# Kernel tuning notes

Measured on AMD Instinct MI355X. Metric: run time of the kernel, lower is better.

Reference implementation:

```python
import jax, jax.numpy as jnp
import numpy as np

N = 1_000_000   # pose-graph nodes
E = 2_000_000   # edges (odometry + loop closures)
M = N - 1
L1, L2, L3, L4 = 1.0, 0.1, 1.0, 0.1  # loss weights
EPS = 1e-8

# ---- quaternion / Lie-group helpers (pypose convention: [x,y,z,w]) ----

def qmul(q, r):
    qv, qw = q[..., :3], q[..., 3:]
    rv, rw = r[..., :3], r[..., 3:]
    w = qw * rw - jnp.sum(qv * rv, axis=-1, keepdims=True)
    v = qw * rv + rw * qv + jnp.cross(qv, rv)
    return jnp.concatenate([v, w], axis=-1)

def qconj(q):  # inverse of a unit quaternion
    return jnp.concatenate([-q[..., :3], q[..., 3:]], axis=-1)

def qrot(q, v):  # rotate vector v by unit quaternion q
    qv, qw = q[..., :3], q[..., 3:]
    t = 2.0 * jnp.cross(qv, v)
    return v + qw * t + jnp.cross(qv, t)

def so3_log(q):  # SO3 -> so3 rotation vector phi
    v, w = q[..., :3], q[..., 3]
    n = jnp.linalg.norm(v, axis=-1)
    theta = 2.0 * jnp.arctan2(n, w)
    big = n > EPS
    k = jnp.where(big, theta / jnp.where(big, n, 1.0), 2.0 / jnp.where(jnp.abs(w) > EPS, w, 1.0))
    return v * k[..., None]

def se3_log(t, q):  # SE3 -> se3 = [tau(3), phi(3)] (translation first, pypose order)
    phi = so3_log(q)
    theta2 = jnp.sum(phi * phi, axis=-1)
    theta = jnp.sqrt(theta2)
    small = theta < 1e-4
    ts = jnp.where(small, 1.0, theta)
    # V^{-1} coefficient: 1/theta^2 - (1+cos)/(2 theta sin); Taylor -> 1/12
    coef = jnp.where(small, 1.0 / 12.0,
                     1.0 / jnp.where(small, 1.0, theta2)
                     - (1.0 + jnp.cos(ts)) / (2.0 * ts * jnp.sin(ts)))
    pxt = jnp.cross(phi, t)
    tau = t - 0.5 * pxt + coef[..., None] * jnp.cross(phi, pxt)  # V^{-1} t without 3x3 mats
    return jnp.concatenate([tau, phi], axis=-1)

def _unit_quat(key, n):
    q = jax.random.normal(key, (n, 4), dtype=jnp.float32)
    return q / jnp.linalg.norm(q, axis=-1, keepdims=True)

def setup_inputs() -> dict:
    key = jax.random.key(0)
    k = jax.random.split(key, 9)
    nodes = jnp.concatenate([jax.random.normal(k[0], (N, 3), jnp.float32), _unit_quat(k[1], N)], axis=-1)
    vels = jax.random.normal(k[2], (N, 3), jnp.float32)
    edges = jax.random.randint(k[3], (E, 2), 0, N, dtype=jnp.int32)
    poses = jnp.concatenate([jax.random.normal(k[4], (E, 3), jnp.float32), _unit_quat(k[5], E)], axis=-1)
    imu_drots = _unit_quat(k[6], M)
    imu_dtrans = 0.1 * jax.random.normal(k[7], (M, 3), jnp.float32)
    imu_dvels = 0.1 * jax.random.normal(k[8], (M, 3), jnp.float32)
    dts = jnp.full((M, 1), 0.05, dtype=jnp.float32)
    return dict(edges=edges, nodes=nodes, vels=vels, poses=poses,
                imu_drots=imu_drots, imu_dtrans=imu_dtrans, imu_dvels=imu_dvels, dts=dts)

def reference(edges, nodes, vels, poses, imu_drots, imu_dtrans, imu_dvels, dts):
    t_n, q_n = nodes[:, :3], nodes[:, 3:]
    # --- pose-graph residual: (poses^-1 o node1^-1 o node2).Log() ---
    n1 = nodes[edges[:, 0]]
    n2 = nodes[edges[:, 1]]
    t1, q1 = n1[:, :3], n1[:, 3:]
    t2, q2 = n2[:, :3], n2[:, 3:]
    tp, qp = poses[:, :3], poses[:, 3:]
    qi1 = qconj(q1)
    ti1 = -qrot(qi1, t1)           # node1^-1
    qa = qmul(qi1, q2)
    ta = ti1 + qrot(qi1, t2)       # node1^-1 o node2
    qip = qconj(qp)
    tip = -qrot(qip, tp)           # poses^-1
    qe = qmul(qip, qa)
    te = tip + qrot(qip, ta)
    pgerr = se3_log(te, qe)                                   # [E, 6]
    # --- adjacent velocity residual ---
    adjvelerr = imu_dvels - (vels[1:] - vels[:-1])            # [M, 3]
    # --- IMU rotation residual: (drot^-1 o R1^-1 o R2).Log() ---
    qre = qmul(qconj(imu_drots), qmul(qconj(q_n[:-1]), q_n[1:]))
    imuroterr = so3_log(qre)                                  # [M, 3]
    # --- translation/velocity residual ---
    transvelerr = (t_n[1:] - t_n[:-1]) - (vels[:-1] * dts + imu_dtrans)  # [M, 3]
    return jnp.concatenate([L1 * pgerr.ravel(), L2 * adjvelerr.ravel(),
                            L3 * imuroterr.ravel(), L4 * transvelerr.ravel()], axis=0)
```

## Files before the change

### kernel.cpp

```cpp
#include <hip/hip_runtime.h>
#include <math.h>

#define EPS_Q 1e-8f

struct F3 { float x, y, z; };
struct Q4 { F3 v; float w; };

__device__ __forceinline__ F3 add3(F3 a, F3 b){ return {a.x+b.x, a.y+b.y, a.z+b.z}; }
__device__ __forceinline__ F3 sub3(F3 a, F3 b){ return {a.x-b.x, a.y-b.y, a.z-b.z}; }
__device__ __forceinline__ F3 scal3(float s, F3 a){ return {s*a.x, s*a.y, s*a.z}; }
__device__ __forceinline__ float dot3(F3 a, F3 b){ return a.x*b.x + a.y*b.y + a.z*b.z; }
__device__ __forceinline__ F3 cross3(F3 a, F3 b){
    return { a.y*b.z - a.z*b.y, a.z*b.x - a.x*b.z, a.x*b.y - a.y*b.x };
}
__device__ __forceinline__ Q4 qmul(Q4 q, Q4 r){
    Q4 o;
    o.w = q.w*r.w - dot3(q.v, r.v);
    o.v = add3(add3(scal3(q.w, r.v), scal3(r.w, q.v)), cross3(q.v, r.v));
    return o;
}
__device__ __forceinline__ Q4 qconj(Q4 q){ return { {-q.v.x, -q.v.y, -q.v.z}, q.w }; }
__device__ __forceinline__ F3 qrot(Q4 q, F3 v){
    F3 t = scal3(2.0f, cross3(q.v, v));
    return add3(add3(v, scal3(q.w, t)), cross3(q.v, t));
}
__device__ __forceinline__ F3 so3_log(Q4 q){
    float n = sqrtf(dot3(q.v, q.v));
    float theta = 2.0f * atan2f(n, q.w);
    float k;
    if (n > EPS_Q) k = theta / n;
    else           k = 2.0f / ((fabsf(q.w) > EPS_Q) ? q.w : 1.0f);
    return scal3(k, q.v);
}

__device__ __forceinline__ void edge_compute(F3 t1, Q4 q1, F3 t2, Q4 q2,
                                             F3 tp, Q4 qp, float* __restrict__ o)
{
    Q4 qi1 = qconj(q1);
    F3 ti1 = scal3(-1.0f, qrot(qi1, t1));
    Q4 qa  = qmul(qi1, q2);
    F3 ta  = add3(ti1, qrot(qi1, t2));

    Q4 qip = qconj(qp);
    F3 tip = scal3(-1.0f, qrot(qip, tp));
    Q4 qe  = qmul(qip, qa);
    F3 te  = add3(tip, qrot(qip, ta));

    F3 phi = so3_log(qe);
    float theta2 = dot3(phi, phi);
    float theta  = sqrtf(theta2);
    float coef;
    if (theta < 1e-4f) {
        coef = 1.0f / 12.0f;
    } else {
        coef = 1.0f / theta2 - (1.0f + cosf(theta)) / (2.0f * theta * sinf(theta));
    }
    F3 pxt = cross3(phi, te);
    F3 tau = add3(sub3(te, scal3(0.5f, pxt)), scal3(coef, cross3(phi, pxt)));

    __builtin_nontemporal_store(tau.x, o + 0);
    __builtin_nontemporal_store(tau.y, o + 1);
    __builtin_nontemporal_store(tau.z, o + 2);
    __builtin_nontemporal_store(phi.x, o + 3);
    __builtin_nontemporal_store(phi.y, o + 4);
    __builtin_nontemporal_store(phi.z, o + 5);
}

__global__ void pad_nodes_kernel(const float* __restrict__ nodes,
                                 float4* __restrict__ pn, int N)
{
    int i = blockIdx.x * blockDim.x + threadIdx.x;
    if (i >= N) return;
    const float* s = nodes + 7*(size_t)i;
    float4 a = { s[0], s[1], s[2], s[3] };
    float4 b = { s[4], s[5], s[6], 0.0f };
    pn[2*(size_t)i    ] = a;
    pn[2*(size_t)i + 1] = b;
}

__global__ void fused_main(const int*    __restrict__ edges,
                           const float4* __restrict__ pn,
                           const float*  __restrict__ poses,
                           const float*  __restrict__ vels,
                           const float*  __restrict__ imu_drots,
                           const float*  __restrict__ imu_dtrans,
                           const float*  __restrict__ imu_dvels,
                           const float*  __restrict__ dts,
                           float*        __restrict__ out,
                           int E, int M, int edge_threads)
{
    int tid = blockIdx.x * blockDim.x + threadIdx.x;
    if (tid < edge_threads) {
        int e0 = 2*tid;
        int e1 = e0 + 1;
        bool has1 = (e1 < E);
        int e1s = has1 ? e1 : e0;

        int i0 = __builtin_nontemporal_load(edges + 2*(size_t)e0);
        int j0 = __builtin_nontemporal_load(edges + 2*(size_t)e0 + 1);
        int i1 = __builtin_nontemporal_load(edges + 2*(size_t)e1s);
        int j1 = __builtin_nontemporal_load(edges + 2*(size_t)e1s + 1);

        float4 na0 = pn[2*(size_t)i0], na1 = pn[2*(size_t)i0 + 1];
        float4 nb0 = pn[2*(size_t)j0], nb1 = pn[2*(size_t)j0 + 1];
        float4 nc0 = pn[2*(size_t)i1], nc1 = pn[2*(size_t)i1 + 1];
        float4 nd0 = pn[2*(size_t)j1], nd1 = pn[2*(size_t)j1 + 1];

        const float* p0 = poses + 7*(size_t)e0;
        const float* p1 = poses + 7*(size_t)e1s;
        float pp0[7], pp1[7];
        #pragma unroll
        for (int k = 0; k < 7; ++k) pp0[k] = __builtin_nontemporal_load(p0 + k);
        #pragma unroll
        for (int k = 0; k < 7; ++k) pp1[k] = __builtin_nontemporal_load(p1 + k);

        {
            F3 t1 = {na0.x, na0.y, na0.z};  Q4 q1 = {{na0.w, na1.x, na1.y}, na1.z};
            F3 t2 = {nb0.x, nb0.y, nb0.z};  Q4 q2 = {{nb0.w, nb1.x, nb1.y}, nb1.z};
            F3 tp = {pp0[0], pp0[1], pp0[2]}; Q4 qp = {{pp0[3], pp0[4], pp0[5]}, pp0[6]};
            edge_compute(t1, q1, t2, q2, tp, qp, out + 6*(size_t)e0);
        }
        if (has1) {
            F3 t1 = {nc0.x, nc0.y, nc0.z};  Q4 q1 = {{nc0.w, nc1.x, nc1.y}, nc1.z};
            F3 t2 = {nd0.x, nd0.y, nd0.z};  Q4 q2 = {{nd0.w, nd1.x, nd1.y}, nd1.z};
            F3 tp = {pp1[0], pp1[1], pp1[2]}; Q4 qp = {{pp1[3], pp1[4], pp1[5]}, pp1[6]};
            edge_compute(t1, q1, t2, q2, tp, qp, out + 6*(size_t)e1);
        }
    } else {
        int m = tid - edge_threads;
        if (m >= M) return;

        const size_t off_adjvel   = 6*(size_t)E;
        const size_t off_imurot   = off_adjvel + 3*(size_t)M;
        const size_t off_transvel = off_imurot + 3*(size_t)M;

        float4 n0a = pn[2*(size_t)m    ], n0b = pn[2*(size_t)m + 1];
        float4 n1a = pn[2*(size_t)m + 2], n1b = pn[2*(size_t)m + 3];
        F3 t0 = {n0a.x, n0a.y, n0a.z};  Q4 q0 = {{n0a.w, n0b.x, n0b.y}, n0b.z};
        F3 t1 = {n1a.x, n1a.y, n1a.z};  Q4 q1 = {{n1a.w, n1b.x, n1b.y}, n1b.z};

        F3 v0 = {vels[3*(size_t)m],     vels[3*(size_t)m + 1], vels[3*(size_t)m + 2]};
        F3 v1 = {vels[3*(size_t)m + 3], vels[3*(size_t)m + 4], vels[3*(size_t)m + 5]};

        F3 dvm = { __builtin_nontemporal_load(imu_dvels + 3*(size_t)m),
                   __builtin_nontemporal_load(imu_dvels + 3*(size_t)m + 1),
                   __builtin_nontemporal_load(imu_dvels + 3*(size_t)m + 2) };
        F3 adjv = sub3(dvm, sub3(v1, v0));
        __builtin_nontemporal_store(0.1f * adjv.x, out + off_adjvel + 3*(size_t)m);
        __builtin_nontemporal_store(0.1f * adjv.y, out + off_adjvel + 3*(size_t)m + 1);
        __builtin_nontemporal_store(0.1f * adjv.z, out + off_adjvel + 3*(size_t)m + 2);

        const float4 drv = ((const float4*)imu_drots)[m];
        Q4 dr = {{drv.x, drv.y, drv.z}, drv.w};
        Q4 qre = qmul(qconj(dr), qmul(qconj(q0), q1));
        F3 rot = so3_log(qre);
        __builtin_nontemporal_store(rot.x, out + off_imurot + 3*(size_t)m);
        __builtin_nontemporal_store(rot.y, out + off_imurot + 3*(size_t)m + 1);
        __builtin_nontemporal_store(rot.z, out + off_imurot + 3*(size_t)m + 2);

        float dt = dts[m];
        F3 dtr = { __builtin_nontemporal_load(imu_dtrans + 3*(size_t)m),
                   __builtin_nontemporal_load(imu_dtrans + 3*(size_t)m + 1),
                   __builtin_nontemporal_load(imu_dtrans + 3*(size_t)m + 2) };
        F3 tv = sub3(sub3(t1, t0), add3(scal3(dt, v0), dtr));
        __builtin_nontemporal_store(0.1f * tv.x, out + off_transvel + 3*(size_t)m);
        __builtin_nontemporal_store(0.1f * tv.y, out + off_transvel + 3*(size_t)m + 1);
        __builtin_nontemporal_store(0.1f * tv.z, out + off_transvel + 3*(size_t)m + 2);
    }
}

__global__ void edge_kernel(const int*   __restrict__ edges,
                            const float* __restrict__ nodes,
                            const float* __restrict__ poses,
                            float*       __restrict__ out,
                            int E)
{
    int e = blockIdx.x * blockDim.x + threadIdx.x;
    if (e >= E) return;
    int i = edges[2*(size_t)e];
    int j = edges[2*(size_t)e + 1];
    const float* n1 = nodes + 7*(size_t)i;
    const float* n2 = nodes + 7*(size_t)j;
    const float* p  = poses + 7*(size_t)e;
    F3 t1 = {n1[0], n1[1], n1[2]};  Q4 q1 = {{n1[3], n1[4], n1[5]}, n1[6]};
    F3 t2 = {n2[0], n2[1], n2[2]};  Q4 q2 = {{n2[3], n2[4], n2[5]}, n2[6]};
    F3 tp = {p[0],  p[1],  p[2]};   Q4 qp = {{p[3],  p[4],  p[5]},  p[6]};
    edge_compute(t1, q1, t2, q2, tp, qp, out + 6*(size_t)e);
}

__global__ void node_kernel(const float* __restrict__ nodes,
                            const float* __restrict__ vels,
                            const float* __restrict__ imu_drots,
                            const float* __restrict__ imu_dtrans,
                            const float* __restrict__ imu_dvels,
                            const float* __restrict__ dts,
                            float*       __restrict__ out,
                            int M,
                            size_t off_adjvel, size_t off_imurot, size_t off_transvel)
{
    int m = blockIdx.x * blockDim.x + threadIdx.x;
    if (m >= M) return;
    const float* n0 = nodes + 7*(size_t)m;
    const float* n1 = nodes + 7*(size_t)(m+1);
    F3 t0 = {n0[0], n0[1], n0[2]};  Q4 q0 = {{n0[3], n0[4], n0[5]}, n0[6]};
    F3 t1 = {n1[0], n1[1], n1[2]};  Q4 q1 = {{n1[3], n1[4], n1[5]}, n1[6]};
    F3 v0 = {vels[3*(size_t)m],     vels[3*(size_t)m + 1], vels[3*(size_t)m + 2]};
    F3 v1 = {vels[3*(size_t)m + 3], vels[3*(size_t)m + 4], vels[3*(size_t)m + 5]};
    F3 dvm = {imu_dvels[3*(size_t)m], imu_dvels[3*(size_t)m + 1], imu_dvels[3*(size_t)m + 2]};
    F3 adjv = sub3(dvm, sub3(v1, v0));
    out[off_adjvel + 3*(size_t)m    ] = 0.1f * adjv.x;
    out[off_adjvel + 3*(size_t)m + 1] = 0.1f * adjv.y;
    out[off_adjvel + 3*(size_t)m + 2] = 0.1f * adjv.z;
    Q4 dr = {{imu_drots[4*(size_t)m], imu_drots[4*(size_t)m + 1], imu_drots[4*(size_t)m + 2]},
              imu_drots[4*(size_t)m + 3]};
    Q4 qre = qmul(qconj(dr), qmul(qconj(q0), q1));
    F3 rot = so3_log(qre);
    out[off_imurot + 3*(size_t)m    ] = rot.x;
    out[off_imurot + 3*(size_t)m + 1] = rot.y;
    out[off_imurot + 3*(size_t)m + 2] = rot.z;
    float dt = dts[m];
    F3 dtr = {imu_dtrans[3*(size_t)m], imu_dtrans[3*(size_t)m + 1], imu_dtrans[3*(size_t)m + 2]};
    F3 tv = sub3(sub3(t1, t0), add3(scal3(dt, v0), dtr));
    out[off_transvel + 3*(size_t)m    ] = 0.1f * tv.x;
    out[off_transvel + 3*(size_t)m + 1] = 0.1f * tv.y;
    out[off_transvel + 3*(size_t)m + 2] = 0.1f * tv.z;
}

extern "C" void kernel_launch(void* const* d_in, const int* in_sizes, int n_in,
                              void* d_out, int out_size, void* d_ws, size_t ws_size,
                              hipStream_t stream) {
    const int*   edges      = (const int*)  d_in[0];
    const float* nodes      = (const float*)d_in[1];
    const float* vels       = (const float*)d_in[2];
    const float* poses      = (const float*)d_in[3];
    const float* imu_drots  = (const float*)d_in[4];
    const float* imu_dtrans = (const float*)d_in[5];
    const float* imu_dvels  = (const float*)d_in[6];
    const float* dts        = (const float*)d_in[7];
    float* out = (float*)d_out;

    const int E = in_sizes[0] / 2;
    const int N = in_sizes[1] / 7;
    const int M = in_sizes[7];

    const int BLK = 256;
    const size_t need = 2 * (size_t)N * sizeof(float4);

    if (ws_size >= need) {
        float4* pn = (float4*)d_ws;
        pad_nodes_kernel<<<(N + BLK - 1) / BLK, BLK, 0, stream>>>(nodes, pn, N);
        const int edge_threads = (E + 1) / 2;
        const long long total = (long long)edge_threads + M;
        fused_main<<<(int)((total + BLK - 1) / BLK), BLK, 0, stream>>>(
            edges, pn, poses, vels, imu_drots, imu_dtrans, imu_dvels, dts,
            out, E, M, edge_threads);
    } else {
        const size_t off_adjvel   = 6*(size_t)E;
        const size_t off_imurot   = off_adjvel + 3*(size_t)M;
        const size_t off_transvel = off_imurot + 3*(size_t)M;
        edge_kernel<<<(E + BLK - 1) / BLK, BLK, 0, stream>>>(edges, nodes, poses, out, E);
        node_kernel<<<(M + BLK - 1) / BLK, BLK, 0, stream>>>(nodes, vels, imu_drots, imu_dtrans,
                                                             imu_dvels, dts, out, M,
                                                             off_adjvel, off_imurot, off_transvel);
    }
}
```

Before: 301.1 us.

## Split fused kernel, interleave edge pairs by half-stride, drop nontemporal hints

Replaces the fused edge/node kernel with separate edge and node kernels. Each edge thread now handles edges t and t+half, so adjacent threads read adjacent edge and pose records. Edge indices are loaded as int2. Nontemporal load and store hints are replaced with ordinary accesses. This aims for better coalescing and simpler per-kernel code, at the cost of an extra launch and possible cache pollution from the output stores.

After: 275.8 us. 8.4% less time.

```diff
diff --git a/kernel.cpp b/kernel.cpp
--- a/kernel.cpp
+++ b/kernel.cpp
@@ -58,12 +58,8 @@
     F3 pxt = cross3(phi, te);
     F3 tau = add3(sub3(te, scal3(0.5f, pxt)), scal3(coef, cross3(phi, pxt)));
 
-    __builtin_nontemporal_store(tau.x, o + 0);
-    __builtin_nontemporal_store(tau.y, o + 1);
-    __builtin_nontemporal_store(tau.z, o + 2);
-    __builtin_nontemporal_store(phi.x, o + 3);
-    __builtin_nontemporal_store(phi.y, o + 4);
-    __builtin_nontemporal_store(phi.z, o + 5);
+    o[0] = tau.x; o[1] = tau.y; o[2] = tau.z;
+    o[3] = phi.x; o[4] = phi.y; o[5] = phi.z;
 }
 
 __global__ void pad_nodes_kernel(const float* __restrict__ nodes,
@@ -78,95 +74,90 @@
     pn[2*(size_t)i + 1] = b;
 }
 
-__global__ void fused_main(const int*    __restrict__ edges,
-                           const float4* __restrict__ pn,
-                           const float*  __restrict__ poses,
-                           const float*  __restrict__ vels,
-                           const float*  __restrict__ imu_drots,
-                           const float*  __restrict__ imu_dtrans,
-                           const float*  __restrict__ imu_dvels,
-                           const float*  __restrict__ dts,
-                           float*        __restrict__ out,
-                           int E, int M, int edge_threads)
-{
-    int tid = blockIdx.x * blockDim.x + threadIdx.x;
-    if (tid < edge_threads) {
-        int e0 = 2*tid;
-        int e1 = e0 + 1;
-        bool has1 = (e1 < E);
-        int e1s = has1 ? e1 : e0;
-
-        int i0 = __builtin_nontemporal_load(edges + 2*(size_t)e0);
-        int j0 = __builtin_nontemporal_load(edges + 2*(size_t)e0 + 1);
-        int i1 = __builtin_nontemporal_load(edges + 2*(size_t)e1s);
-        int j1 = __builtin_nontemporal_load(edges + 2*(size_t)e1s + 1);
-
-        float4 na0 = pn[2*(size_t)i0], na1 = pn[2*(size_t)i0 + 1];
-        float4 nb0 = pn[2*(size_t)j0], nb1 = pn[2*(size_t)j0 + 1];
-        float4 nc0 = pn[2*(size_t)i1], nc1 = pn[2*(size_t)i1 + 1];
-        float4 nd0 = pn[2*(size_t)j1], nd1 = pn[2*(size_t)j1 + 1];
-
-        const float* p0 = poses + 7*(size_t)e0;
-        const float* p1 = poses + 7*(size_t)e1s;
-        float pp0[7], pp1[7];
-        #pragma unroll
-        for (int k = 0; k < 7; ++k) pp0[k] = __builtin_nontemporal_load(p0 + k);
-        #pragma unroll
-        for (int k = 0; k < 7; ++k) pp1[k] = __builtin_nontemporal_load(p1 + k);
-
-        {
-            F3 t1 = {na0.x, na0.y, na0.z};  Q4 q1 = {{na0.w, na1.x, na1.y}, na1.z};
-            F3 t2 = {nb0.x, nb0.y, nb0.z};  Q4 q2 = {{nb0.w, nb1.x, nb1.y}, nb1.z};
-            F3 tp = {pp0[0], pp0[1], pp0[2]}; Q4 qp = {{pp0[3], pp0[4], pp0[5]}, pp0[6]};
-            edge_compute(t1, q1, t2, q2, tp, qp, out + 6*(size_t)e0);
-        }
-        if (has1) {
-            F3 t1 = {nc0.x, nc0.y, nc0.z};  Q4 q1 = {{nc0.w, nc1.x, nc1.y}, nc1.z};
-            F3 t2 = {nd0.x, nd0.y, nd0.z};  Q4 q2 = {{nd0.w, nd1.x, nd1.y}, nd1.z};
-            F3 tp = {pp1[0], pp1[1], pp1[2]}; Q4 qp = {{pp1[3], pp1[4], pp1[5]}, pp1[6]};
-            edge_compute(t1, q1, t2, q2, tp, qp, out + 6*(size_t)e1);
-        }
-    } else {
-        int m = tid - edge_threads;
-        if (m >= M) return;
-
-        const size_t off_adjvel   = 6*(size_t)E;
-        const size_t off_imurot   = off_adjvel + 3*(size_t)M;
-        const size_t off_transvel = off_imurot + 3*(size_t)M;
-
-        float4 n0a = pn[2*(size_t)m    ], n0b = pn[2*(size_t)m + 1];
-        float4 n1a = pn[2*(size_t)m + 2], n1b = pn[2*(size_t)m + 3];
-        F3 t0 = {n0a.x, n0a.y, n0a.z};  Q4 q0 = {{n0a.w, n0b.x, n0b.y}, n0b.z};
-        F3 t1 = {n1a.x, n1a.y, n1a.z};  Q4 q1 = {{n1a.w, n1b.x, n1b.y}, n1b.z};
-
-        F3 v0 = {vels[3*(size_t)m],     vels[3*(size_t)m + 1], vels[3*(size_t)m + 2]};
-        F3 v1 = {vels[3*(size_t)m + 3], vels[3*(size_t)m + 4], vels[3*(size_t)m + 5]};
-
-        F3 dvm = { __builtin_nontemporal_load(imu_dvels + 3*(size_t)m),
-                   __builtin_nontemporal_load(imu_dvels + 3*(size_t)m + 1),
-                   __builtin_nontemporal_load(imu_dvels + 3*(size_t)m + 2) };
-        F3 adjv = sub3(dvm, sub3(v1, v0));
-        __builtin_nontemporal_store(0.1f * adjv.x, out + off_adjvel + 3*(size_t)m);
-        __builtin_nontemporal_store(0.1f * adjv.y, out + off_adjvel + 3*(size_t)m + 1);
-        __builtin_nontemporal_store(0.1f * adjv.z, out + off_adjvel + 3*(size_t)m + 2);
-
-        const float4 drv = ((const float4*)imu_drots)[m];
-        Q4 dr = {{drv.x, drv.y, drv.z}, drv.w};
-        Q4 qre = qmul(qconj(dr), qmul(qconj(q0), q1));
-        F3 rot = so3_log(qre);
-        __builtin_nontemporal_store(rot.x, out + off_imurot + 3*(size_t)m);
-        __builtin_nontemporal_store(rot.y, out + off_imurot + 3*(size_t)m + 1);
-        __builtin_nontemporal_store(rot.z, out + off_imurot + 3*(size_t)m + 2);
-
-        float dt = dts[m];
-        F3 dtr = { __builtin_nontemporal_load(imu_dtrans + 3*(size_t)m),
-                   __builtin_nontemporal_load(imu_dtrans + 3*(size_t)m + 1),
-                   __builtin_nontemporal_load(imu_dtrans + 3*(size_t)m + 2) };
-        F3 tv = sub3(sub3(t1, t0), add3(scal3(dt, v0), dtr));
-        __builtin_nontemporal_store(0.1f * tv.x, out + off_transvel + 3*(size_t)m);
-        __builtin_nontemporal_store(0.1f * tv.y, out + off_transvel + 3*(size_t)m + 1);
-        __builtin_nontemporal_store(0.1f * tv.z, out + off_transvel + 3*(size_t)m + 2);
-    }
+__global__ void edge_kernel2(const int2*   __restrict__ edges,
+                             const float4* __restrict__ pn,
+                             const float*  __restrict__ poses,
+                             float*        __restrict__ out,
+                             int E, int half)
+{
+    int t = blockIdx.x * blockDim.x + threadIdx.x;
+    if (t >= half) return;
+    int e0 = t;
+    int e1 = t + half;
+    bool has1 = (e1 < E);
+    int e1s = has1 ? e1 : e0;
+
+    int2 ab0 = edges[e0];
+    int2 ab1 = edges[e1s];
+
+    float4 na0 = pn[2*(size_t)ab0.x], na1 = pn[2*(size_t)ab0.x + 1];
+    float4 nb0 = pn[2*(size_t)ab0.y], nb1 = pn[2*(size_t)ab0.y + 1];
+    float4 nc0 = pn[2*(size_t)ab1.x], nc1 = pn[2*(size_t)ab1.x + 1];
+    float4 nd0 = pn[2*(size_t)ab1.y], nd1 = pn[2*(size_t)ab1.y + 1];
+
+    const float* p0 = poses + 7*(size_t)e0;
+    const float* p1 = poses + 7*(size_t)e1s;
+    float pp0[7], pp1[7];
+    #pragma unroll
+    for (int k = 0; k < 7; ++k) pp0[k] = p0[k];
+    #pragma unroll
+    for (int k = 0; k < 7; ++k) pp1[k] = p1[k];
+
+    {
+        F3 t1 = {na0.x, na0.y, na0.z};  Q4 q1 = {{na0.w, na1.x, na1.y}, na1.z};
+        F3 t2 = {nb0.x, nb0.y, nb0.z};  Q4 q2 = {{nb0.w, nb1.x, nb1.y}, nb1.z};
+        F3 tp = {pp0[0], pp0[1], pp0[2]}; Q4 qp = {{pp0[3], pp0[4], pp0[5]}, pp0[6]};
+        edge_compute(t1, q1, t2, q2, tp, qp, out + 6*(size_t)e0);
+    }
+    if (has1) {
+        F3 t1 = {nc0.x, nc0.y, nc0.z};  Q4 q1 = {{nc0.w, nc1.x, nc1.y}, nc1.z};
+        F3 t2 = {nd0.x, nd0.y, nd0.z};  Q4 q2 = {{nd0.w, nd1.x, nd1.y}, nd1.z};
+        F3 tp = {pp1[0], pp1[1], pp1[2]}; Q4 qp = {{pp1[3], pp1[4], pp1[5]}, pp1[6]};
+        edge_compute(t1, q1, t2, q2, tp, qp, out + 6*(size_t)e1);
+    }
+}
+
+__global__ void node_kernel(const float4* __restrict__ pn,
+                            const float*  __restrict__ vels,
+                            const float4* __restrict__ imu_drots,
+                            const float*  __restrict__ imu_dtrans,
+                            const float*  __restrict__ imu_dvels,
+                            const float*  __restrict__ dts,
+                            float*        __restrict__ out,
+                            int M,
+                            size_t off_adjvel, size_t off_imurot, size_t off_transvel)
+{
+    int m = blockIdx.x * blockDim.x + threadIdx.x;
+    if (m >= M) return;
+
+    float4 n0a = pn[2*(size_t)m    ], n0b = pn[2*(size_t)m + 1];
+    float4 n1a = pn[2*(size_t)m + 2], n1b = pn[2*(size_t)m + 3];
+    F3 t0 = {n0a.x, n0a.y, n0a.z};  Q4 q0 = {{n0a.w, n0b.x, n0b.y}, n0b.z};
+    F3 t1 = {n1a.x, n1a.y, n1a.z};  Q4 q1 = {{n1a.w, n1b.x, n1b.y}, n1b.z};
+
+    F3 v0 = {vels[3*(size_t)m],     vels[3*(size_t)m + 1], vels[3*(size_t)m + 2]};
+    F3 v1 = {vels[3*(size_t)m + 3], vels[3*(size_t)m + 4], vels[3*(size_t)m + 5]};
+
+    F3 dvm = {imu_dvels[3*(size_t)m], imu_dvels[3*(size_t)m + 1], imu_dvels[3*(size_t)m + 2]};
+    F3 adjv = sub3(dvm, sub3(v1, v0));
+    out[off_adjvel + 3*(size_t)m    ] = 0.1f * adjv.x;
+    out[off_adjvel + 3*(size_t)m + 1] = 0.1f * adjv.y;
+    out[off_adjvel + 3*(size_t)m + 2] = 0.1f * adjv.z;
+
+    float4 drv = imu_drots[m];
+    Q4 dr = {{drv.x, drv.y, drv.z}, drv.w};
+    Q4 qre = qmul(qconj(dr), qmul(qconj(q0), q1));
+    F3 rot = so3_log(qre);
+    out[off_imurot + 3*(size_t)m    ] = rot.x;
+    out[off_imurot + 3*(size_t)m + 1] = rot.y;
+    out[off_imurot + 3*(size_t)m + 2] = rot.z;
+
+    float dt = dts[m];
+    F3 dtr = {imu_dtrans[3*(size_t)m], imu_dtrans[3*(size_t)m + 1], imu_dtrans[3*(size_t)m + 2]};
+    F3 tv = sub3(sub3(t1, t0), add3(scal3(dt, v0), dtr));
+    out[off_transvel + 3*(size_t)m    ] = 0.1f * tv.x;
+    out[off_transvel + 3*(size_t)m + 1] = 0.1f * tv.y;
+    out[off_transvel + 3*(size_t)m + 2] = 0.1f * tv.z;
 }
 
 __global__ void edge_kernel(const int*   __restrict__ edges,
@@ -188,15 +179,15 @@
     edge_compute(t1, q1, t2, q2, tp, qp, out + 6*(size_t)e);
 }
 
-__global__ void node_kernel(const float* __restrict__ nodes,
-                            const float* __restrict__ vels,
-                            const float* __restrict__ imu_drots,
-                            const float* __restrict__ imu_dtrans,
-                            const float* __restrict__ imu_dvels,
-                            const float* __restrict__ dts,
-                            float*       __restrict__ out,
-                            int M,
-                            size_t off_adjvel, size_t off_imurot, size_t off_transvel)
+__global__ void node_kernel_raw(const float* __restrict__ nodes,
+                                const float* __restrict__ vels,
+                                const float* __restrict__ imu_drots,
+                                const float* __restrict__ imu_dtrans,
+                                const float* __restrict__ imu_dvels,
+                                const float* __restrict__ dts,
+                                float*       __restrict__ out,
+                                int M,
+                                size_t off_adjvel, size_t off_imurot, size_t off_transvel)
 {
     int m = blockIdx.x * blockDim.x + threadIdx.x;
     if (m >= M) return;
@@ -243,24 +234,26 @@
     const int N = in_sizes[1] / 7;
     const int M = in_sizes[7];
 
+    const size_t off_adjvel   = 6*(size_t)E;
+    const size_t off_imurot   = off_adjvel + 3*(size_t)M;
+    const size_t off_transvel = off_imurot + 3*(size_t)M;
+
     const int BLK = 256;
     const size_t need = 2 * (size_t)N * sizeof(float4);
 
     if (ws_size >= need) {
         float4* pn = (float4*)d_ws;
         pad_nodes_kernel<<<(N + BLK - 1) / BLK, BLK, 0, stream>>>(nodes, pn, N);
-        const int edge_threads = (E + 1) / 2;
-        const long long total = (long long)edge_threads + M;
-        fused_main<<<(int)((total + BLK - 1) / BLK), BLK, 0, stream>>>(
-            edges, pn, poses, vels, imu_drots, imu_dtrans, imu_dvels, dts,
-            out, E, M, edge_threads);
+        const int half = (E + 1) / 2;
+        edge_kernel2<<<(half + BLK - 1) / BLK, BLK, 0, stream>>>(
+            (const int2*)edges, pn, poses, out, E, half);
+        node_kernel<<<(M + BLK - 1) / BLK, BLK, 0, stream>>>(
+            pn, vels, (const float4*)imu_drots, imu_dtrans, imu_dvels, dts, out, M,
+            off_adjvel, off_imurot, off_transvel);
     } else {
-        const size_t off_adjvel   = 6*(size_t)E;
-        const size_t off_imurot   = off_adjvel + 3*(size_t)M;
-        const size_t off_transvel = off_imurot + 3*(size_t)M;
         edge_kernel<<<(E + BLK - 1) / BLK, BLK, 0, stream>>>(edges, nodes, poses, out, E);
-        node_kernel<<<(M + BLK - 1) / BLK, BLK, 0, stream>>>(nodes, vels, imu_drots, imu_dtrans,
-                                                             imu_dvels, dts, out, M,
-                                                             off_adjvel, off_imurot, off_transvel);
-    }
-}
+        node_kernel_raw<<<(M + BLK - 1) / BLK, BLK, 0, stream>>>(nodes, vels, imu_drots, imu_dtrans,
+                                                                 imu_dvels, dts, out, M,
+                                                                 off_adjvel, off_imurot, off_transvel);
+    }
+}
```
